# Performance work log

Measured on AMD Instinct MI355X. Metric: run time of the kernel, lower is better.

The kernel has to match this reference:

```python
import jax, jax.numpy as jnp
import numpy as np

B, C, N, O, K = 4, 64, 8192, 128, 20


def setup_inputs() -> dict:
    key = jax.random.key(0)
    k1, k2, k3 = jax.random.split(key, 3)
    x = jax.random.normal(k1, (B, C, N), dtype=jnp.float32)
    # Conv2d(2C, 2C, 1, bias=False) weight squeezed to [2C, 2C]
    W1 = jax.random.normal(k2, (2 * C, 2 * C), dtype=jnp.float32) * (1.0 / np.sqrt(2 * C))
    # Conv2d(2C, O, 1, bias=False) weight squeezed to [O, 2C]
    W2 = jax.random.normal(k3, (O, 2 * C), dtype=jnp.float32) * (1.0 / np.sqrt(2 * C))
    return {"x": x, "W1": W1, "W2": W2, "spiral_size": K}


def _knn_idx(x, k):
    # x: [B, C, N]; negative squared pairwise distance, top-k = k nearest (incl. self)
    inner = -2.0 * jnp.einsum('bcn,bcm->bnm', x, x)          # [B, N, N]
    xx = jnp.sum(x * x, axis=1)                               # [B, N]
    pd = -xx[:, :, None] - inner - xx[:, None, :]             # [B, N, N]
    return jax.lax.top_k(pd, k)[1]                            # [B, N, k] int32


def reference(x, W1, W2, spiral_size):
    b, c, n = x.shape
    idx = _knn_idx(x, spiral_size)                            # [B, N, K]
    xt = jnp.transpose(x, (0, 2, 1))                          # [B, N, C]
    spirals = xt[jnp.arange(b)[:, None, None], idx]           # [B, N, K, C] neighbor gather
    center = jnp.broadcast_to(xt[:, :, None, :], spirals.shape)
    feats = jnp.concatenate([spirals - center, center], axis=-1)  # [B, N, K, 2C]
    h = jnp.einsum('bnkc,dc->bnkd', feats, W1)                # 1x1 conv1
    gate = jax.nn.softmax(h, axis=2)                          # softmax over neighbor dim K
    gated = feats * gate                                      # [B, N, K, 2C]
    out = jnp.einsum('bnkc,oc->bon', gated, W2)               # conv2 + sum over K -> [B, O, N]
    return out
```

## Files before the change

kernel.cpp:

```cpp
#include <hip/hip_runtime.h>
#include <math.h>

#define BB 4
#define CC 64
#define NN 8192
#define OO 128
#define KK 20
#define DD 128
#define BUFSZ 25

typedef short bf16x8 __attribute__((ext_vector_type(8)));
typedef float f32x4 __attribute__((ext_vector_type(4)));
typedef unsigned short u16x8 __attribute__((ext_vector_type(8)));
typedef unsigned long long u64;

typedef __attribute__((address_space(1))) const void gvoid;
typedef __attribute__((address_space(3))) void lvoid;

__device__ __forceinline__ u64 packkey(float v, int idx) {
  unsigned u = __float_as_uint(v);
  unsigned o = ((int)u < 0) ? ~u : (u | 0x80000000u);
  return (((u64)o) << 32) | (unsigned)(~idx);
}
__device__ __forceinline__ float keyval(u64 k) {
  unsigned o = (unsigned)(k >> 32);
  unsigned u = (o & 0x80000000u) ? (o ^ 0x80000000u) : ~o;
  return __uint_as_float(u);
}
#define INITKEY (((u64)0x007FFFFFu) << 32)

__device__ __forceinline__ unsigned short bf_rne(float f) {
  unsigned u = __float_as_uint(f);
  u += 0x7FFFu + ((u >> 16) & 1u);
  return (unsigned short)(u >> 16);
}
__device__ __forceinline__ float bf_f(unsigned short h) {
  return __uint_as_float(((unsigned)h) << 16);
}

__global__ __launch_bounds__(128) void prep_kernel(const float* __restrict__ x,
                                                   float* __restrict__ xx,
                                                   unsigned short* __restrict__ xs) {
  const int tid = threadIdx.x;
  const int b = blockIdx.y;
  const int n0 = blockIdx.x * 128;
  const float* xb = x + (size_t)b * CC * NN;
  float xv[CC];
  float acc = 0.0f;
  #pragma unroll
  for (int c = 0; c < CC; ++c) {
    float v = xb[(size_t)c * NN + n0 + tid];
    acc += v * v;
    xv[c] = v;
  }
  xx[b * NN + n0 + tid] = acc;

  const int n = n0 + tid;
  char* xsrow = ((char*)xs) + ((size_t)b * NN + n) * 384;
  const int swn = (n & 7) << 4;
  #pragma unroll
  for (int gr = 0; gr < 8; ++gr) {
    u16x8 h8, m8, l8;
    #pragma unroll
    for (int e = 0; e < 8; ++e) {
      float v = xv[gr * 8 + e];
      unsigned short h = bf_rne(v);
      float r = v - bf_f(h);
      unsigned short m = bf_rne(r);
      r -= bf_f(m);
      unsigned short l = bf_rne(r);
      h8[e] = (unsigned short)h; m8[e] = m; l8[e] = l;
    }
    *(u16x8*)(xsrow + (((gr * 16) + 0) ^ swn)) = h8;
    *(u16x8*)(xsrow + (((gr * 16) + 128) ^ swn)) = m8;
    *(u16x8*)(xsrow + (((gr * 16) + 256) ^ swn)) = l8;
  }
}

__global__ __launch_bounds__(256, 2) void knn_kernel(
    const unsigned short* __restrict__ xs, const float* __restrict__ xx,
    int* __restrict__ fidx) {
  __shared__ unsigned short atile[64 * 192];
  __shared__ float cxx[64];
  __shared__ u64 abuf[4][64][BUFSZ];

  const int tid = threadIdx.x;
  const int w = tid >> 6;
  const int lane = tid & 63;
  const int r = lane & 15;
  const int g = lane >> 4;
  const int b = blockIdx.y;
  const int qbase = blockIdx.x * 64 + w * 16;
  const int q = qbase + r;
  const char* xsb = ((const char*)xs) + (size_t)b * NN * 384;

  bf16x8 bq[3][2];
  {
    const char* qrow = xsb + (size_t)q * 384;
    const int sw = (q & 7) << 4;
    #pragma unroll
    for (int s = 0; s < 3; ++s)
      #pragma unroll
      for (int c = 0; c < 2; ++c)
        bq[s][c] = *(const bf16x8*)(qrow + ((s * 128 + c * 64 + g * 16) ^ sw));
  }
  const float xxq = xx[b * NN + q];

  u64 tk[KK];
  #pragma unroll
  for (int j = 0; j < KK; ++j) tk[j] = INITKEY;
  float minv = -INFINITY;
  int cnt = 0;
  u64* mybuf = &abuf[w][lane][0];

  for (int t = 0; t < NN / 64; ++t) {
    {
      const char* src = xsb + (size_t)t * 64 * 384;
      #pragma unroll
      for (int it = 0; it < 6; ++it) {
        __builtin_amdgcn_global_load_lds(
            (gvoid*)(src + it * 4096 + tid * 16),
            (lvoid*)(((char*)atile) + it * 4096 + tid * 16), 16, 0, 0);
      }
      if (tid < 16) {
        __builtin_amdgcn_global_load_lds(
            (gvoid*)(xx + b * NN + t * 64 + tid * 4),
            (lvoid*)(cxx + tid * 4), 16, 0, 0);
      }
    }
    __syncthreads();

    #pragma unroll
    for (int ct = 0; ct < 4; ++ct) {
      const char* arow = ((const char*)atile) + (ct * 16 + r) * 384;
      const int sw = (r & 7) << 4;
      bf16x8 a6[6];
      #pragma unroll
      for (int c6 = 0; c6 < 6; ++c6)
        a6[c6] = *(const bf16x8*)(arow + ((c6 * 64 + g * 16) ^ sw));
      f32x4 acc = {0.f, 0.f, 0.f, 0.f};
      #pragma unroll
      for (int s = 2; s >= 0; --s)
        #pragma unroll
        for (int c6 = 0; c6 < 6; ++c6)
          acc = __builtin_amdgcn_mfma_f32_16x16x32_bf16(a6[c6], bq[s][c6 & 1],
                                                        acc, 0, 0, 0);
      #pragma unroll
      for (int j = 0; j < 4; ++j) {
        const int ml = ct * 16 + g * 4 + j;
        float pd = (-xxq - (-2.0f * acc[j])) - cxx[ml];
        if (pd > minv) { mybuf[cnt] = packkey(pd, t * 64 + ml); ++cnt; }
      }
    }
    __syncthreads();

    if (__any(cnt > BUFSZ - 16)) {
      int mxc = cnt;
      #pragma unroll
      for (int o = 32; o > 0; o >>= 1) {
        int v = __shfl_xor(mxc, o);
        mxc = mxc > v ? mxc : v;
      }
      for (int i = 0; i < mxc; ++i) {
        u64 k = (i < cnt) ? mybuf[i] : 0ULL;
        if (k > tk[KK - 1]) {
          #pragma unroll
          for (int jj = KK - 1; jj >= 1; --jj)
            tk[jj] = (k > tk[jj - 1]) ? tk[jj - 1] : ((k > tk[jj]) ? k : tk[jj]);
          tk[0] = (k > tk[0]) ? k : tk[0];
        }
      }
      cnt = 0;
      minv = keyval(tk[KK - 1]);
    }
  }

  {
    int mxc = cnt;
    #pragma unroll
    for (int o = 32; o > 0; o >>= 1) {
      int v = __shfl_xor(mxc, o);
      mxc = mxc > v ? mxc : v;
    }
    for (int i = 0; i < mxc; ++i) {
      u64 k = (i < cnt) ? mybuf[i] : 0ULL;
      if (k > tk[KK - 1]) {
        #pragma unroll
        for (int jj = KK - 1; jj >= 1; --jj)
          tk[jj] = (k > tk[jj - 1]) ? tk[jj - 1] : ((k > tk[jj]) ? k : tk[jj]);
        tk[0] = (k > tk[0]) ? k : tk[0];
      }
    }
  }

  u64* ml = &abuf[w][0][0];
  #pragma unroll
  for (int j = 0; j < KK; ++j) ml[lane * KK + j] = tk[j];
  __syncthreads();
  if (lane < 16) {
    int* fo = fidx + ((size_t)b * NN + qbase + lane) * KK;
    const u64* L0 = ml + (lane + 0) * KK;
    const u64* L1 = ml + (lane + 16) * KK;
    const u64* L2 = ml + (lane + 32) * KK;
    const u64* L3 = ml + (lane + 48) * KK;
    int p0 = 0, p1 = 0, p2 = 0, p3 = 0;
    u64 h0 = L0[0], h1 = L1[0], h2 = L2[0], h3 = L3[0];
    #pragma unroll
    for (int k = 0; k < KK; ++k) {
      u64 bv = h0; int bc = 0;
      if (h1 > bv) { bv = h1; bc = 1; }
      if (h2 > bv) { bv = h2; bc = 2; }
      if (h3 > bv) { bv = h3; bc = 3; }
      fo[k] = (int)(~(unsigned)bv);
      if (bc == 0)      { ++p0; h0 = (p0 < KK) ? L0[p0] : 0ULL; }
      else if (bc == 1) { ++p1; h1 = (p1 < KK) ? L1[p1] : 0ULL; }
      else if (bc == 2) { ++p2; h2 = (p2 < KK) ? L2[p2] : 0ULL; }
      else              { ++p3; h3 = (p3 < KK) ? L3[p3] : 0ULL; }
    }
  }
}

__global__ __launch_bounds__(256) void w1prep_kernel(const float* __restrict__ W1,
                                                     unsigned short* __restrict__ w1p) {
  for (int e = threadIdx.x; e < 12288; e += 256) {
    const int f = e >> 9;
    const int rr = e & 511;
    const int l = rr >> 3;
    const int j = rr & 7;
    const int pair = f / 3, s = f % 3;
    const int dt = pair >> 1, kc = pair & 1;
    const int d = dt * 16 + (l & 15);
    const int c = kc * 32 + (l >> 4) * 8 + j;
    const float v = W1[d * DD + c];
    const unsigned short h = bf_rne(v);
    float r = v - bf_f(h);
    const unsigned short m = bf_rne(r);
    r -= bf_f(m);
    const unsigned short lo = bf_rne(r);
    w1p[(size_t)f * 512 + l * 8 + j] = (s == 0) ? h : ((s == 1) ? m : lo);
  }
}

#define MFMA16(A, B, C) __builtin_amdgcn_mfma_f32_16x16x32_bf16((A), (B), (C), 0, 0, 0)

template <int SA, int SB>
__device__ __forceinline__ void h_term(const bf16x8 (&a)[3][2][2],
                                       const bf16x8 (&w1f)[24],
                                       f32x4 (&acc)[4][2]) {
  #pragma unroll
  for (int dt = 0; dt < 4; ++dt)
    #pragma unroll
    for (int kc = 0; kc < 2; ++kc) {
      const bf16x8 bf = w1f[(dt * 2 + kc) * 3 + SB];
      acc[dt][0] = MFMA16(a[SA][kc][0], bf, acc[dt][0]);
      acc[dt][1] = MFMA16(a[SA][kc][1], bf, acc[dt][1]);
    }
}

template <int DT>
__device__ __forceinline__ float d1_epi(const bf16x8 (&a)[3][2][2],
                                        bf16x8 id0, bf16x8 id1,
                                        const f32x4 (&acc)[4][2], int g) {
  constexpr int KC = DT >> 1;
  const bf16x8 idp = (DT & 1) ? id1 : id0;
  f32x4 yf0 = {0.f, 0.f, 0.f, 0.f}, yf1 = {0.f, 0.f, 0.f, 0.f};
  yf0 = MFMA16(a[1][KC][0], idp, yf0);
  yf0 = MFMA16(a[0][KC][0], idp, yf0);
  yf1 = MFMA16(a[1][KC][1], idp, yf1);
  yf1 = MFMA16(a[0][KC][1], idp, yf1);
  const f32x4 h0 = acc[DT][0], h1 = acc[DT][1];
  float mx = fmaxf(fmaxf(h0[0], h0[1]), fmaxf(h0[2], h0[3]));
  mx = fmaxf(mx, fmaxf(fmaxf(h1[0], h1[1]), fmaxf(h1[2], h1[3])));
  mx = fmaxf(mx, __shfl_xor(mx, 16));
  mx = fmaxf(mx, __shfl_xor(mx, 32));
  float sl = 0.f, tl = 0.f;
  #pragma unroll
  for (int j = 0; j < 4; ++j) {
    const float e = __expf(h0[j] - mx);
    sl += e; tl += yf0[j] * e;
  }
  if (g == 0) {
    #pragma unroll
    for (int j = 0; j < 4; ++j) {
      const float e = __expf(h1[j] - mx);
      sl += e; tl += yf1[j] * e;
    }
  }
  sl += __shfl_xor(sl, 16); sl += __shfl_xor(sl, 32);
  tl += __shfl_xor(tl, 16); tl += __shfl_xor(tl, 32);
  return tl / sl;
}

__global__ __launch_bounds__(256, 2) void d1_kernel(
    const unsigned short* __restrict__ xs, const int* __restrict__ fidx,
    const unsigned short* __restrict__ w1p, float* __restrict__ gbuf) {
  const int tid = threadIdx.x;
  const int w = tid >> 6;
  const int lane = tid & 63;
  const int r = lane & 15;
  const int g = lane >> 4;
  const int b = blockIdx.y;
  const char* xsb = ((const char*)xs) + (size_t)b * NN * 384;

  bf16x8 w1f[24];
  #pragma unroll
  for (int f = 0; f < 24; ++f)
    w1f[f] = *(const bf16x8*)(((const char*)w1p) + f * 1024 + lane * 16);

  bf16x8 id0, id1;
  #pragma unroll
  for (int j = 0; j < 8; ++j) {
    id0[j] = (g == (r >> 3) && j == (r & 7)) ? (short)0x3F80 : (short)0;
    id1[j] = (g == 2 + (r >> 3) && j == (r & 7)) ? (short)0x3F80 : (short)0;
  }

  for (int i = 0; i < 4; ++i) {
    const int n = blockIdx.x * 16 + w * 4 + i;
    const size_t ng = (size_t)b * NN + n;
    const int* kp = fidx + ng * KK;
    const int row0 = kp[r];
    const int row1 = kp[16 + (r & 3)];
    const char* rp0 = xsb + (size_t)row0 * 384;
    const char* rp1 = xsb + (size_t)row1 * 384;
    const int sw0 = (row0 & 7) << 4, sw1 = (row1 & 7) << 4;

    bf16x8 a[3][2][2];
    #pragma unroll
    for (int s = 0; s < 3; ++s)
      #pragma unroll
      for (int kc = 0; kc < 2; ++kc) {
        const int off = s * 128 + kc * 64 + g * 16;
        a[s][kc][0] = *(const bf16x8*)(rp0 + (off ^ sw0));
        a[s][kc][1] = *(const bf16x8*)(rp1 + (off ^ sw1));
      }

    const char* zrow = xsb + (size_t)n * 384;
    const int swn = (n & 7) << 4;
    float zl;
    {
      const unsigned short zh = *(const unsigned short*)(zrow + ((2 * lane) ^ swn));
      const unsigned short zm = *(const unsigned short*)(zrow + ((128 + 2 * lane) ^ swn));
      const unsigned short zo = *(const unsigned short*)(zrow + ((256 + 2 * lane) ^ swn));
      zl = bf_f(zh) + bf_f(zm) + bf_f(zo);
    }

    f32x4 acc[4][2];
    #pragma unroll
    for (int dt = 0; dt < 4; ++dt) {
      acc[dt][0] = (f32x4){0.f, 0.f, 0.f, 0.f};
      acc[dt][1] = (f32x4){0.f, 0.f, 0.f, 0.f};
    }
    h_term<2, 0>(a, w1f, acc);
    h_term<0, 2>(a, w1f, acc);
    h_term<1, 1>(a, w1f, acc);
    h_term<1, 0>(a, w1f, acc);
    h_term<0, 1>(a, w1f, acc);
    h_term<0, 0>(a, w1f, acc);

    const float t0 = d1_epi<0>(a, id0, id1, acc, g);
    const float t1 = d1_epi<1>(a, id0, id1, acc, g);
    const float t2 = d1_epi<2>(a, id0, id1, acc, g);
    const float t3 = d1_epi<3>(a, id0, id1, acc, g);

    float* go = gbuf + ng * DD;
    go[64 + lane] = zl;
    const float z0 = __shfl(zl, r);
    const float z1 = __shfl(zl, 16 + r);
    const float z2 = __shfl(zl, 32 + r);
    const float z3 = __shfl(zl, 48 + r);
    if (lane < 16) {
      go[r]      = t0 - z0;
      go[16 + r] = t1 - z1;
      go[32 + r] = t2 - z2;
      go[48 + r] = t3 - z3;
    }
  }
}

__global__ __launch_bounds__(256) void d2_kernel(const float* __restrict__ gbuf,
                                                 const float* __restrict__ W2,
                                                 float* __restrict__ out) {
  __shared__ float4 w2s[OO * 32];
  const int tid = threadIdx.x;
  const int b = blockIdx.y;
  const int n0 = blockIdx.x * 32;
  const float4* w2v = (const float4*)W2;
  for (int t = tid; t < OO * 32; t += 256) {
    int o = t >> 5, c4 = t & 31;
    w2s[o * 32 + (c4 ^ (o & 7))] = w2v[t];
  }
  __syncthreads();
  const int og = tid & 7;
  const int ni = tid >> 3;
  const int n = n0 + ni;
  const float4* gp = (const float4*)(gbuf + ((size_t)b * NN + n) * DD);
  float acc[16];
  #pragma unroll
  for (int j = 0; j < 16; ++j) acc[j] = 0.0f;
  for (int c4 = 0; c4 < 32; ++c4) {
    float4 g4 = gp[c4];
    #pragma unroll
    for (int j = 0; j < 16; ++j) {
      const int o = j * 8 + og;
      float4 w4 = w2s[o * 32 + (c4 ^ og)];
      acc[j] += g4.x * w4.x + g4.y * w4.y + g4.z * w4.z + g4.w * w4.w;
    }
  }
  float* outb = out + (size_t)b * OO * NN;
  #pragma unroll
  for (int j = 0; j < 16; ++j) {
    outb[(size_t)(j * 8 + og) * NN + n] = acc[j];
  }
}

extern "C" void kernel_launch(void* const* d_in, const int* in_sizes, int n_in,
                              void* d_out, int out_size, void* d_ws, size_t ws_size,
                              hipStream_t stream) {
  const float* x  = (const float*)d_in[0];
  const float* W1 = (const float*)d_in[1];
  const float* W2 = (const float*)d_in[2];
  float* out = (float*)d_out;
  char* ws = (char*)d_ws;
  unsigned short* xs = (unsigned short*)(ws);
  float* xx = (float*)(ws + 12582912);
  unsigned short* w1p = (unsigned short*)(ws + 12582912);
  int* fidx = (int*)(ws + 12713984);
  float* gbuf = (float*)(ws + 15335424);

  prep_kernel<<<dim3(NN / 128, BB), 128, 0, stream>>>(x, xx, xs);
  knn_kernel<<<dim3(NN / 64, BB), 256, 0, stream>>>(xs, xx, fidx);
  w1prep_kernel<<<dim3(1), 256, 0, stream>>>(W1, w1p);
  d1_kernel<<<dim3(NN / 16, BB), 256, 0, stream>>>(xs, fidx, w1p, gbuf);
  d2_kernel<<<dim3(NN / 32, BB), 256, 0, stream>>>(gbuf, W2, out);
}
```

Baseline: 805.0 us.

## Double-buffer KNN tile loads and flush candidate buffer every half tile

Makes the LDS tile and norm buffers double-buffered so the next 64-column tile is prefetched with global_load_lds while the current tile is being processed, and removes one barrier per iteration. The candidate buffer shrinks from 25 to 15 entries and is flushed into the top-k list after each half tile, which frees LDS, possibly for higher occupancy. MFMA sections are wrapped in s_setprio to favour matrix issue. The trade-off is more frequent top-k rebuild checks and reuse of atile for the final merge scratch.

```diff
diff --git a/kernel.cpp b/kernel.cpp
--- a/kernel.cpp
+++ b/kernel.cpp
@@ -7,7 +7,7 @@
 #define OO 128
 #define KK 20
 #define DD 128
-#define BUFSZ 25
+#define BUFSZ 15
 
 typedef short bf16x8 __attribute__((ext_vector_type(8)));
 typedef float f32x4 __attribute__((ext_vector_type(4)));
@@ -80,10 +80,9 @@
 __global__ __launch_bounds__(256, 2) void knn_kernel(
     const unsigned short* __restrict__ xs, const float* __restrict__ xx,
     int* __restrict__ fidx) {
-  __shared__ unsigned short atile[64 * 192];
-  __shared__ float cxx[64];
+  __shared__ __attribute__((aligned(16))) unsigned short atile[2][64 * 192];
+  __shared__ float cxx[2][64];
   __shared__ u64 abuf[4][64][BUFSZ];
-
   const int tid = threadIdx.x;
   const int w = tid >> 6;
   const int lane = tid & 63;
@@ -113,69 +112,23 @@
   int cnt = 0;
   u64* mybuf = &abuf[w][lane][0];
 
-  for (int t = 0; t < NN / 64; ++t) {
-    {
-      const char* src = xsb + (size_t)t * 64 * 384;
-      #pragma unroll
-      for (int it = 0; it < 6; ++it) {
-        __builtin_amdgcn_global_load_lds(
-            (gvoid*)(src + it * 4096 + tid * 16),
-            (lvoid*)(((char*)atile) + it * 4096 + tid * 16), 16, 0, 0);
-      }
-      if (tid < 16) {
-        __builtin_amdgcn_global_load_lds(
-            (gvoid*)(xx + b * NN + t * 64 + tid * 4),
-            (lvoid*)(cxx + tid * 4), 16, 0, 0);
-      }
-    }
-    __syncthreads();
-
-    #pragma unroll
-    for (int ct = 0; ct < 4; ++ct) {
-      const char* arow = ((const char*)atile) + (ct * 16 + r) * 384;
-      const int sw = (r & 7) << 4;
-      bf16x8 a6[6];
-      #pragma unroll
-      for (int c6 = 0; c6 < 6; ++c6)
-        a6[c6] = *(const bf16x8*)(arow + ((c6 * 64 + g * 16) ^ sw));
-      f32x4 acc = {0.f, 0.f, 0.f, 0.f};
-      #pragma unroll
-      for (int s = 2; s >= 0; --s)
-        #pragma unroll
-        for (int c6 = 0; c6 < 6; ++c6)
-          acc = __builtin_amdgcn_mfma_f32_16x16x32_bf16(a6[c6], bq[s][c6 & 1],
-                                                        acc, 0, 0, 0);
-      #pragma unroll
-      for (int j = 0; j < 4; ++j) {
-        const int ml = ct * 16 + g * 4 + j;
-        float pd = (-xxq - (-2.0f * acc[j])) - cxx[ml];
-        if (pd > minv) { mybuf[cnt] = packkey(pd, t * 64 + ml); ++cnt; }
-      }
-    }
-    __syncthreads();
-
-    if (__any(cnt > BUFSZ - 16)) {
-      int mxc = cnt;
-      #pragma unroll
-      for (int o = 32; o > 0; o >>= 1) {
-        int v = __shfl_xor(mxc, o);
-        mxc = mxc > v ? mxc : v;
-      }
-      for (int i = 0; i < mxc; ++i) {
-        u64 k = (i < cnt) ? mybuf[i] : 0ULL;
-        if (k > tk[KK - 1]) {
-          #pragma unroll
-          for (int jj = KK - 1; jj >= 1; --jj)
-            tk[jj] = (k > tk[jj - 1]) ? tk[jj - 1] : ((k > tk[jj]) ? k : tk[jj]);
-          tk[0] = (k > tk[0]) ? k : tk[0];
-        }
-      }
-      cnt = 0;
-      minv = keyval(tk[KK - 1]);
-    }
-  }
-
-  {
+  auto stage = [&](int t, int p) {
+    const char* src = xsb + (size_t)t * 64 * 384;
+    char* dst = (char*)atile[p];
+    #pragma unroll
+    for (int it = 0; it < 6; ++it) {
+      __builtin_amdgcn_global_load_lds(
+          (gvoid*)(src + it * 4096 + tid * 16),
+          (lvoid*)(dst + it * 4096 + tid * 16), 16, 0, 0);
+    }
+    if (tid < 16) {
+      __builtin_amdgcn_global_load_lds(
+          (gvoid*)(xx + b * NN + t * 64 + tid * 4),
+          (lvoid*)(cxx[p] + tid * 4), 16, 0, 0);
+    }
+  };
+
+  auto rebuild = [&]() {
     int mxc = cnt;
     #pragma unroll
     for (int o = 32; o > 0; o >>= 1) {
@@ -191,9 +144,52 @@
         tk[0] = (k > tk[0]) ? k : tk[0];
       }
     }
-  }
-
-  u64* ml = &abuf[w][0][0];
+    cnt = 0;
+    minv = keyval(tk[KK - 1]);
+  };
+
+  stage(0, 0);
+  __syncthreads();
+
+  for (int t = 0; t < NN / 64; ++t) {
+    const int p = t & 1;
+    if (t < NN / 64 - 1) stage(t + 1, p ^ 1);
+
+    #pragma unroll
+    for (int half = 0; half < 2; ++half) {
+      #pragma unroll
+      for (int cth = 0; cth < 2; ++cth) {
+        const int ct = half * 2 + cth;
+        const char* arow = ((const char*)atile[p]) + (ct * 16 + r) * 384;
+        const int sw = (r & 7) << 4;
+        bf16x8 a6[6];
+        #pragma unroll
+        for (int c6 = 0; c6 < 6; ++c6)
+          a6[c6] = *(const bf16x8*)(arow + ((c6 * 64 + g * 16) ^ sw));
+        f32x4 acc = {0.f, 0.f, 0.f, 0.f};
+        __builtin_amdgcn_s_setprio(1);
+        #pragma unroll
+        for (int s = 2; s >= 0; --s)
+          #pragma unroll
+          for (int c6 = 0; c6 < 6; ++c6)
+            acc = __builtin_amdgcn_mfma_f32_16x16x32_bf16(a6[c6], bq[s][c6 & 1],
+                                                          acc, 0, 0, 0);
+        __builtin_amdgcn_s_setprio(0);
+        #pragma unroll
+        for (int j = 0; j < 4; ++j) {
+          const int ml = ct * 16 + g * 4 + j;
+          float pd = (-xxq - (-2.0f * acc[j])) - cxx[p][ml];
+          if (pd > minv) { mybuf[cnt] = packkey(pd, t * 64 + ml); ++cnt; }
+        }
+      }
+      if (__any(cnt > 7)) rebuild();
+    }
+    __syncthreads();
+  }
+
+  rebuild();
+
+  u64* ml = ((u64*)&atile[0][0]) + (size_t)w * 64 * KK;
   #pragma unroll
   for (int j = 0; j < KK; ++j) ml[lane * KK + j] = tk[j];
   __syncthreads();
```

Measured after the change: 791.2 us. Within noise of the previous version (-1.7%).
